# Performance work log

Measured on AMD Instinct MI355X. Metric: run time of the kernel, lower is better.

## Reference

```python
import jax, jax.numpy as jnp
import numpy as np

TROPICAL_ZERO = jnp.float32(-1e38)  # tropical additive identity (acts as -inf)


def setup_inputs() -> dict:
    key = jax.random.key(0)
    k_x, k_w = jax.random.split(key)
    B, IN, OUT = 4096, 256, 256
    x = jax.random.normal(k_x, (B, IN), dtype=jnp.float32)
    # weight = log(rand + 1e-6), matching nn.Parameter init in the torch module
    weight = jnp.log(jax.random.uniform(k_w, (OUT, IN), dtype=jnp.float32) + 1e-6)
    bias = jnp.zeros((OUT,), dtype=jnp.float32)
    return {"x": x, "weight": weight, "bias": bias}


def reference(x, weight, bias):
    # Tropical (max-plus) matmul: out[b, j] = max_k (x[b, k] + w[j, k]) + bias[j]
    # restricted to 'non-tropical-zero' products; if all products are tropical
    # zero, the output stays TROPICAL_ZERO (no bias added), as in the torch loop.
    products = x[:, None, :] + weight[None, :, :]          # [B, out, in]
    mask = products > TROPICAL_ZERO                        # [B, out, in]
    masked = jnp.where(mask, products, -jnp.inf)
    max_val = jnp.max(masked, axis=-1)                     # [B, out]
    any_valid = jnp.any(mask, axis=-1)                     # [B, out]
    out = jnp.where(any_valid, max_val + bias[None, :], TROPICAL_ZERO)
    return out
```

## Files before the change

kernel.cpp:

```cpp
#include <hip/hip_runtime.h>


#define TZERO -1e38f

constexpr int K    = 256;
constexpr int N    = 256;
constexpr int ROWS = 16;
constexpr int COLS = 128;
constexpr int NT   = 512;
constexpr int KSEG = 32;

__global__ __launch_bounds__(NT, 4)
void tropical_kernel(const float* __restrict__ x, const float* __restrict__ w,
                     const float* __restrict__ bias, float* __restrict__ out)
{
    __shared__ float part[8][ROWS][COLS];

    const int t    = threadIdx.x;
    const int lane = t & 63;
    const int ws   = __builtin_amdgcn_readfirstlane(t >> 6);
    const int row0 = blockIdx.x * ROWS;
    const int col0 = blockIdx.y * COLS;

    const float* w0 = w + (size_t)(col0 + lane) * K + ws * KSEG;
    const float* w1 = w0 + (size_t)64 * K;
    float4 wA[8], wB[8];
#pragma unroll
    for (int i = 0; i < 8; ++i) {
        wA[i] = *reinterpret_cast<const float4*>(w0 + 4 * i);
        wB[i] = *reinterpret_cast<const float4*>(w1 + 4 * i);
    }

    const float* xbase = x + (size_t)row0 * K;

#pragma unroll 1
    for (int r = 0; r < ROWS; ++r) {
        int off = r * K + ws * KSEG;
        asm("" : "+v"(off));
        const float* xr = xbase + off;

        float a0 = -__builtin_inff();
        float a1 = -__builtin_inff();
#pragma unroll
        for (int i = 0; i < 8; ++i) {
            const float4 xv = *reinterpret_cast<const float4*>(xr + 4 * i);
            const float s0 = xv.x + wA[i].x;
            const float s1 = xv.y + wA[i].y;
            const float s2 = xv.z + wA[i].z;
            const float s3 = xv.w + wA[i].w;
            a0 = fmaxf(fmaxf(a0, s0), s1);
            a0 = fmaxf(fmaxf(a0, s2), s3);
            const float u0 = xv.x + wB[i].x;
            const float u1 = xv.y + wB[i].y;
            const float u2 = xv.z + wB[i].z;
            const float u3 = xv.w + wB[i].w;
            a1 = fmaxf(fmaxf(a1, u0), u1);
            a1 = fmaxf(fmaxf(a1, u2), u3);
        }
        part[ws][r][lane]      = a0;
        part[ws][r][64 + lane] = a1;
    }

    __syncthreads();

    {
        const int c  = t & 127;
        const int rb = t >> 7;
        const float bj = bias[col0 + c];
#pragma unroll
        for (int j = 0; j < 4; ++j) {
            const int r = rb + 4 * j;
            float v = part[0][r][c];
#pragma unroll
            for (int s = 1; s < 8; ++s) v = fmaxf(v, part[s][r][c]);
            out[(size_t)(row0 + r) * N + col0 + c] = (v > TZERO) ? v + bj : TZERO;
        }
    }
}

extern "C" void kernel_launch(void* const* d_in, const int* in_sizes, int n_in,
                              void* d_out, int out_size, void* d_ws, size_t ws_size,
                              hipStream_t stream) {
    const float* x  = (const float*)d_in[0];
    const float* w  = (const float*)d_in[1];
    const float* b  = (const float*)d_in[2];
    float* out      = (float*)d_out;

    dim3 grid(4096 / ROWS, N / COLS);
    tropical_kernel<<<grid, NT, 0, stream>>>(x, w, b, out);
}
```

Baseline: 81.63 us.

## Transpose weights for coalesced loads and double-buffer x rows in tropical kernel

Result: faster. 72.25 us (-11.5%).

```diff
diff --git a/kernel.cpp b/kernel.cpp
--- a/kernel.cpp
+++ b/kernel.cpp
@@ -10,8 +10,55 @@
 constexpr int NT   = 512;
 constexpr int KSEG = 32;
 
-__global__ __launch_bounds__(NT, 4)
-void tropical_kernel(const float* __restrict__ x, const float* __restrict__ w,
+__global__ __launch_bounds__(256)
+void transpose_w(const float* __restrict__ w, float* __restrict__ wT)
+{
+    __shared__ float ls[64][65];
+    const int bi = blockIdx.x * 64;
+    const int bj = blockIdx.y * 64;
+    const int t  = threadIdx.x;
+    const int lr = t >> 4;
+    const int lc = (t & 15) * 4;
+
+#pragma unroll
+    for (int i = 0; i < 4; ++i) {
+        const int r = lr + i * 16;
+        const float4 v =
+            *reinterpret_cast<const float4*>(w + (size_t)(bi + r) * K + bj + lc);
+        ls[r][lc + 0] = v.x; ls[r][lc + 1] = v.y;
+        ls[r][lc + 2] = v.z; ls[r][lc + 3] = v.w;
+    }
+    __syncthreads();
+#pragma unroll
+    for (int i = 0; i < 4; ++i) {
+        const int kk = lr + i * 16;
+        float4 v;
+        v.x = ls[lc + 0][kk]; v.y = ls[lc + 1][kk];
+        v.z = ls[lc + 2][kk]; v.w = ls[lc + 3][kk];
+        *reinterpret_cast<float4*>(wT + (size_t)(bj + kk) * N + bi + lc) = v;
+    }
+}
+
+__device__ __forceinline__ void row_compute(
+    const float4 (&buf)[8], const float (&wA)[KSEG], const float (&wB)[KSEG],
+    float& a0, float& a1)
+{
+    float p0 = -__builtin_inff(), p1 = -__builtin_inff();
+    float q0 = -__builtin_inff(), q1 = -__builtin_inff();
+#pragma unroll
+    for (int i = 0; i < 8; ++i) {
+        const float4 xv = buf[i];
+        p0 = fmaxf(fmaxf(p0, xv.x + wA[4 * i + 0]), xv.y + wA[4 * i + 1]);
+        p1 = fmaxf(fmaxf(p1, xv.z + wA[4 * i + 2]), xv.w + wA[4 * i + 3]);
+        q0 = fmaxf(fmaxf(q0, xv.x + wB[4 * i + 0]), xv.y + wB[4 * i + 1]);
+        q1 = fmaxf(fmaxf(q1, xv.z + wB[4 * i + 2]), xv.w + wB[4 * i + 3]);
+    }
+    a0 = fmaxf(p0, p1);
+    a1 = fmaxf(q0, q1);
+}
+
+__global__ __launch_bounds__(NT, 2)
+void tropical_kernel(const float* __restrict__ x, const float* __restrict__ wT,
                      const float* __restrict__ bias, float* __restrict__ out)
 {
     __shared__ float part[8][ROWS][COLS];
@@ -22,43 +69,44 @@
     const int row0 = blockIdx.x * ROWS;
     const int col0 = blockIdx.y * COLS;
 
-    const float* w0 = w + (size_t)(col0 + lane) * K + ws * KSEG;
-    const float* w1 = w0 + (size_t)64 * K;
-    float4 wA[8], wB[8];
+    const int k0 = ws * KSEG;
+    float wA[KSEG], wB[KSEG];
+    {
+        const float* wp = wT + (size_t)k0 * N + col0 + lane;
 #pragma unroll
-    for (int i = 0; i < 8; ++i) {
-        wA[i] = *reinterpret_cast<const float4*>(w0 + 4 * i);
-        wB[i] = *reinterpret_cast<const float4*>(w1 + 4 * i);
+        for (int k = 0; k < KSEG; ++k) {
+            wA[k] = wp[(size_t)k * N];
+            wB[k] = wp[(size_t)k * N + 64];
+        }
     }
 
-    const float* xbase = x + (size_t)row0 * K;
+    const float* xp = x + (size_t)row0 * K + k0;
 
+    float4 bA[8], bB[8];
+#pragma unroll
+    for (int i = 0; i < 8; ++i)
+        bA[i] = *reinterpret_cast<const float4*>(xp + 4 * i);
+
+    float a0, a1;
 #pragma unroll 1
-    for (int r = 0; r < ROWS; ++r) {
-        int off = r * K + ws * KSEG;
-        asm("" : "+v"(off));
-        const float* xr = xbase + off;
+    for (int r = 0; r < ROWS; r += 2) {
+#pragma unroll
+        for (int i = 0; i < 8; ++i)
+            bB[i] = *reinterpret_cast<const float4*>(xp + (r + 1) * K + 4 * i);
 
-        float a0 = -__builtin_inff();
-        float a1 = -__builtin_inff();
-#pragma unroll
-        for (int i = 0; i < 8; ++i) {
-            const float4 xv = *reinterpret_cast<const float4*>(xr + 4 * i);
-            const float s0 = xv.x + wA[i].x;
-            const float s1 = xv.y + wA[i].y;
-            const float s2 = xv.z + wA[i].z;
-            const float s3 = xv.w + wA[i].w;
-            a0 = fmaxf(fmaxf(a0, s0), s1);
-            a0 = fmaxf(fmaxf(a0, s2), s3);
-            const float u0 = xv.x + wB[i].x;
-            const float u1 = xv.y + wB[i].y;
-            const float u2 = xv.z + wB[i].z;
-            const float u3 = xv.w + wB[i].w;
-            a1 = fmaxf(fmaxf(a1, u0), u1);
-            a1 = fmaxf(fmaxf(a1, u2), u3);
-        }
+        row_compute(bA, wA, wB, a0, a1);
         part[ws][r][lane]      = a0;
         part[ws][r][64 + lane] = a1;
+
+        if (r + 2 < ROWS) {
+#pragma unroll
+            for (int i = 0; i < 8; ++i)
+                bA[i] = *reinterpret_cast<const float4*>(xp + (r + 2) * K + 4 * i);
+        }
+
+        row_compute(bB, wA, wB, a0, a1);
+        part[ws][r + 1][lane]      = a0;
+        part[ws][r + 1][64 + lane] = a1;
     }
 
     __syncthreads();
@@ -85,7 +133,11 @@
     const float* w  = (const float*)d_in[1];
     const float* b  = (const float*)d_in[2];
     float* out      = (float*)d_out;
+    float* wT       = (float*)d_ws;
+
+    dim3 tg(4, 4);
+    transpose_w<<<tg, 256, 0, stream>>>(w, wT);
 
     dim3 grid(4096 / ROWS, N / COLS);
-    tropical_kernel<<<grid, NT, 0, stream>>>(x, w, b, out);
+    tropical_kernel<<<grid, NT, 0, stream>>>(x, wT, b, out);
 }
```
